# Kernel tuning notes

Measured on AMD Instinct MI355X. Metric: run time of the kernel, lower is better.

## Reference

```python
import jax, jax.numpy as jnp
import numpy as np

N_NODES = 100000
N_EDGES = 1600000
IN_DIM = 256
HID = 64
HEADS = 2
OUT_DIM = 256
NEG_SLOPE = 0.2  # DGL GATConv default


def setup_inputs() -> dict:
    key = jax.random.key(0)
    ks = jax.random.split(key, 10)
    feat = jax.random.normal(ks[0], (N_NODES, IN_DIM), dtype=jnp.float32)
    src = jax.random.randint(ks[1], (N_EDGES,), 0, N_NODES)
    dst = jax.random.randint(ks[2], (N_EDGES,), 0, N_NODES)
    W = jax.random.normal(ks[3], (IN_DIM, HEADS * HID), dtype=jnp.float32) * 0.05
    attn_l = jax.random.normal(ks[4], (HEADS, HID), dtype=jnp.float32) * 0.05
    attn_r = jax.random.normal(ks[5], (HEADS, HID), dtype=jnp.float32) * 0.05
    gat_bias = jnp.zeros((HEADS * HID,), dtype=jnp.float32)
    lin_W = jax.random.normal(ks[6], (HEADS * HID, OUT_DIM), dtype=jnp.float32) * 0.05
    lin_b = jnp.zeros((OUT_DIM,), dtype=jnp.float32)
    return {"feat": feat, "src": src, "dst": dst, "W": W, "attn_l": attn_l,
            "attn_r": attn_r, "gat_bias": gat_bias, "lin_W": lin_W, "lin_b": lin_b}


def reference(feat, src, dst, W, attn_l, attn_r, gat_bias, lin_W, lin_b):
    N = feat.shape[0]
    H, D = attn_l.shape
    # GATConv: linear projection -> [N, H, D]
    h = (feat @ W).reshape(N, H, D)
    el = jnp.sum(h * attn_l[None], axis=-1)  # [N, H]
    er = jnp.sum(h * attn_r[None], axis=-1)  # [N, H]
    # per-edge attention logits, LeakyReLU
    e = jax.nn.leaky_relu(el[src] + er[dst], NEG_SLOPE)  # [E, H]
    # edge softmax over incoming edges of each dst node
    m = jax.ops.segment_max(e, dst, num_segments=N)      # [N, H] (-inf for isolated nodes, unused)
    ee = jnp.exp(e - m[dst])
    s = jax.ops.segment_sum(ee, dst, num_segments=N)
    alpha = ee / s[dst]                                   # [E, H]
    # weighted aggregation: scatter-add messages to dst
    out = jax.ops.segment_sum(alpha[:, :, None] * h[src], dst, num_segments=N)  # [N, H, D]
    out = out + gat_bias.reshape(1, H, D)
    out = jax.nn.relu(out.reshape(N, H * D))
    return jax.nn.relu(out @ lin_W + lin_b)
```

## Files before the change

kernel.cpp:

```cpp
#include <hip/hip_runtime.h>

#define N_NODES 100000
#define N_EDGES 1600000
#define IN_DIM 256
#define HID 64
#define HEADS 2
#define HD 128
#define OUT_DIM 256
#define NEG_SLOPE 0.2f

typedef unsigned int uint32;
typedef unsigned short ushort16;
typedef __attribute__((ext_vector_type(8))) short bf16x8;
typedef __attribute__((ext_vector_type(4))) float f32x4;

__device__ __forceinline__ ushort16 f2bf(float f) {
    union { float f; uint32 u; } v; v.f = f;
    uint32 u = v.u;
    return (ushort16)((u + 0x7FFFu + ((u >> 16) & 1u)) >> 16);
}
__device__ __forceinline__ float bf2f(ushort16 b) {
    union { uint32 u; float f; } v; v.u = ((uint32)b) << 16;
    return v.f;
}
__device__ __forceinline__ float bflo(uint32 u) {
    union { uint32 u; float f; } v; v.u = u << 16;
    return v.f;
}
__device__ __forceinline__ float bfhi(uint32 u) {
    union { uint32 u; float f; } v; v.u = u & 0xffff0000u;
    return v.f;
}

__global__ __launch_bounds__(256)
void conv_w1(const float* __restrict__ W, ushort16* __restrict__ Wt)
{
    int idx = blockIdx.x * 256 + threadIdx.x;
    int n = idx >> 8, k = idx & 255;
    Wt[idx] = f2bf(W[k * HD + n]);
}
__global__ __launch_bounds__(256)
void conv_w2(const float* __restrict__ W, ushort16* __restrict__ Wt)
{
    int idx = blockIdx.x * 256 + threadIdx.x;
    int n = idx >> 7, k = idx & 127;
    Wt[idx] = f2bf(W[k * OUT_DIM + n]);
}

__global__ __launch_bounds__(256)
void gemm1_mfma(const float* __restrict__ A, const ushort16* __restrict__ Bt,
                ushort16* __restrict__ C, int M)
{
    __shared__ char alds[2 * 16384];
    const int t    = threadIdx.x;
    const int lane = t & 63;
    const int w    = t >> 6;
    const int wr   = w >> 1, wc = w & 1;
    const int m0   = blockIdx.x * 128;
    const int l15  = lane & 15;
    const int lq   = lane >> 4;

    f32x4 acc[4][4] = {};
    float4 av[8];

#define G1_LOAD(KT)                                                               \
    {                                                                             \
        _Pragma("unroll")                                                         \
        for (int i = 0; i < 8; i++) {                                             \
            int flat = t + i * 256;                                               \
            int r = flat >> 4, kq = (flat & 15) * 4;                              \
            int gr = m0 + r; if (gr >= M) gr = M - 1;                             \
            av[i] = *reinterpret_cast<const float4*>(                             \
                        &A[(size_t)gr * IN_DIM + (KT) * 64 + kq]);                \
        }                                                                         \
    }
#define G1_WRITE(BUF)                                                             \
    {                                                                             \
        _Pragma("unroll")                                                         \
        for (int i = 0; i < 8; i++) {                                             \
            int flat = t + i * 256;                                               \
            int r = flat >> 4, kq = (flat & 15) * 4;                              \
            uint2 p;                                                              \
            p.x = (uint32)f2bf(av[i].x) | ((uint32)f2bf(av[i].y) << 16);          \
            p.y = (uint32)f2bf(av[i].z) | ((uint32)f2bf(av[i].w) << 16);          \
            int byte = (r * 128 + kq * 2) ^ ((r & 7) << 4);                       \
            *reinterpret_cast<uint2*>(&alds[(BUF) * 16384 + byte]) = p;           \
        }                                                                         \
    }

    G1_LOAD(0); G1_WRITE(0);
    __syncthreads();
    int cur = 0;
    for (int kt = 0; kt < 4; kt++) {
        if (kt < 3) G1_LOAD(kt + 1);
        bf16x8 bfr[2][4];
#pragma unroll
        for (int ks = 0; ks < 2; ks++)
#pragma unroll
            for (int nf = 0; nf < 4; nf++) {
                int col = wc * 64 + nf * 16 + l15;
                int kb  = (kt * 2 + ks) * 32 + lq * 8;
                bfr[ks][nf] = *reinterpret_cast<const bf16x8*>(&Bt[(size_t)col * 256 + kb]);
            }
#pragma unroll
        for (int ks = 0; ks < 2; ks++) {
            bf16x8 afr[4];
#pragma unroll
            for (int mf = 0; mf < 4; mf++) {
                int row  = wr * 64 + mf * 16 + l15;
                int byte = (row * 128 + ks * 64 + lq * 16) ^ ((row & 7) << 4);
                afr[mf] = *reinterpret_cast<const bf16x8*>(&alds[cur * 16384 + byte]);
            }
#pragma unroll
            for (int mf = 0; mf < 4; mf++)
#pragma unroll
                for (int nf = 0; nf < 4; nf++)
                    acc[mf][nf] = __builtin_amdgcn_mfma_f32_16x16x32_bf16(
                        afr[mf], bfr[ks][nf], acc[mf][nf], 0, 0, 0);
        }
        if (kt < 3) G1_WRITE(cur ^ 1);
        __syncthreads();
        cur ^= 1;
    }
#pragma unroll
    for (int mf = 0; mf < 4; mf++)
#pragma unroll
        for (int nf = 0; nf < 4; nf++)
#pragma unroll
            for (int q = 0; q < 4; q++) {
                int row = m0 + wr * 64 + mf * 16 + lq * 4 + q;
                int col = wc * 64 + nf * 16 + l15;
                if (row < M) C[(size_t)row * HD + col] = f2bf(acc[mf][nf][q]);
            }
#undef G1_LOAD
#undef G1_WRITE
}

__global__ __launch_bounds__(256)
void gemm2_mfma(const ushort16* __restrict__ Ahi, const ushort16* __restrict__ Alo,
                const ushort16* __restrict__ Bt, const float* __restrict__ bias,
                float* __restrict__ Cout, int M)
{
    __shared__ char alds[2 * 32768];
    const int t    = threadIdx.x;
    const int lane = t & 63;
    const int w    = t >> 6;
    const int wr   = w >> 1, wc = w & 1;
    const int m0   = blockIdx.x * 128;
    const int n0   = blockIdx.y * 128;
    const int l15  = lane & 15;
    const int lq   = lane >> 4;

    f32x4 acc[4][4] = {};

#pragma unroll
    for (int p = 0; p < 2; p++) {
        const ushort16* src = p ? Alo : Ahi;
#pragma unroll
        for (int i = 0; i < 8; i++) {
            int flat = t + i * 256;
            int r = flat >> 4, e8 = (flat & 15) * 8;
            int gr = m0 + r; if (gr >= M) gr = M - 1;
            uint4 v = *reinterpret_cast<const uint4*>(&src[(size_t)gr * HD + e8]);
            int byte = (r * 256 + e8 * 2) ^ ((r & 7) << 4);
            *reinterpret_cast<uint4*>(&alds[p * 32768 + byte]) = v;
        }
    }
    bf16x8 bfr[4][4];
#pragma unroll
    for (int ks = 0; ks < 4; ks++)
#pragma unroll
        for (int nf = 0; nf < 4; nf++) {
            int col = n0 + wc * 64 + nf * 16 + l15;
            int kb  = ks * 32 + lq * 8;
            bfr[ks][nf] = *reinterpret_cast<const bf16x8*>(&Bt[(size_t)col * HD + kb]);
        }
    __syncthreads();

#pragma unroll
    for (int pass = 0; pass < 2; pass++) {
#pragma unroll
        for (int ks = 0; ks < 4; ks++) {
            bf16x8 afr[4];
#pragma unroll
            for (int mf = 0; mf < 4; mf++) {
                int row  = wr * 64 + mf * 16 + l15;
                int byte = (row * 256 + ks * 64 + lq * 16) ^ ((row & 7) << 4);
                afr[mf] = *reinterpret_cast<const bf16x8*>(&alds[pass * 32768 + byte]);
            }
#pragma unroll
            for (int mf = 0; mf < 4; mf++)
#pragma unroll
                for (int nf = 0; nf < 4; nf++)
                    acc[mf][nf] = __builtin_amdgcn_mfma_f32_16x16x32_bf16(
                        afr[mf], bfr[ks][nf], acc[mf][nf], 0, 0, 0);
        }
    }

    float bias_v[4];
#pragma unroll
    for (int nf = 0; nf < 4; nf++) bias_v[nf] = bias[n0 + wc * 64 + nf * 16 + l15];
#pragma unroll
    for (int mf = 0; mf < 4; mf++)
#pragma unroll
        for (int nf = 0; nf < 4; nf++)
#pragma unroll
            for (int q = 0; q < 4; q++) {
                int row = m0 + wr * 64 + mf * 16 + lq * 4 + q;
                int col = n0 + wc * 64 + nf * 16 + l15;
                if (row < M)
                    Cout[(size_t)row * OUT_DIM + col] = fmaxf(acc[mf][nf][q] + bias_v[nf], 0.f);
            }
}

__global__ __launch_bounds__(256)
void elr_kernel(const ushort16* __restrict__ hb, const float* __restrict__ attn_l,
                const float* __restrict__ attn_r, float* __restrict__ el,
                float* __restrict__ er)
{
    int w    = (int)((blockIdx.x * blockDim.x + threadIdx.x) >> 6);
    int lane = threadIdx.x & 63;
    if (w >= N_NODES) return;
    float h0 = bf2f(hb[(size_t)w * HD + lane]);
    float h1 = bf2f(hb[(size_t)w * HD + 64 + lane]);
    float v0 = h0 * attn_l[lane];
    float v1 = h1 * attn_l[64 + lane];
    float v2 = h0 * attn_r[lane];
    float v3 = h1 * attn_r[64 + lane];
#pragma unroll
    for (int o = 32; o; o >>= 1) {
        v0 += __shfl_xor(v0, o);
        v1 += __shfl_xor(v1, o);
        v2 += __shfl_xor(v2, o);
        v3 += __shfl_xor(v3, o);
    }
    if (lane == 0) {
        el[w * 2 + 0] = v0; el[w * 2 + 1] = v1;
        er[w * 2 + 0] = v2; er[w * 2 + 1] = v3;
    }
}

__global__ void deg_kernel(const int* __restrict__ dst, int* __restrict__ deg)
{
    int i = blockIdx.x * blockDim.x + threadIdx.x;
    if (i < N_EDGES) atomicAdd(&deg[dst[i]], 1);
}

#define SCAN_B 1024
#define SCAN_NB ((N_NODES + SCAN_B - 1) / SCAN_B)

__global__ __launch_bounds__(SCAN_B)
void scan_part(const int* __restrict__ deg, int* __restrict__ row_ptr,
               int* __restrict__ bsum)
{
    __shared__ int sdata[SCAN_B];
    const int t = threadIdx.x, b = blockIdx.x;
    const int i = b * SCAN_B + t;
    int v = (i < N_NODES) ? deg[i] : 0;
    sdata[t] = v;
    __syncthreads();
    for (int off = 1; off < SCAN_B; off <<= 1) {
        int x = 0;
        if (t >= off) x = sdata[t - off];
        __syncthreads();
        sdata[t] += x;
        __syncthreads();
    }
    if (i < N_NODES) row_ptr[i] = sdata[t] - v;
    if (t == SCAN_B - 1) bsum[b] = sdata[t];
}

__global__ __launch_bounds__(128)
void scan_top(int* __restrict__ bsum, int* __restrict__ row_ptr)
{
    __shared__ int sdata[128];
    const int t = threadIdx.x;
    int v = (t < SCAN_NB) ? bsum[t] : 0;
    sdata[t] = v;
    __syncthreads();
    for (int off = 1; off < 128; off <<= 1) {
        int x = 0;
        if (t >= off) x = sdata[t - off];
        __syncthreads();
        sdata[t] += x;
        __syncthreads();
    }
    if (t < SCAN_NB) bsum[t] = sdata[t] - v;
    if (t == 127) row_ptr[N_NODES] = sdata[127];
}

__global__ __launch_bounds__(SCAN_B)
void scan_add(int* __restrict__ row_ptr, const int* __restrict__ bsum)
{
    const int i = blockIdx.x * SCAN_B + threadIdx.x;
    if (i < N_NODES) row_ptr[i] += bsum[blockIdx.x];
}

__global__ void scatter_kernel(const int* __restrict__ src, const int* __restrict__ dst,
                               const int* __restrict__ row_ptr, int* __restrict__ cursor,
                               int* __restrict__ sorted_src)
{
    int i = blockIdx.x * blockDim.x + threadIdx.x;
    if (i < N_EDGES) {
        int d = dst[i];
        int p = row_ptr[d] + atomicAdd(&cursor[d], 1);
        sorted_src[p] = src[i];
    }
}

__global__ __launch_bounds__(256)
void node_kernel(const ushort16* __restrict__ hb, const float* __restrict__ el,
                 const float* __restrict__ er, const int* __restrict__ row_ptr,
                 const int* __restrict__ sorted_src, float* __restrict__ ws_e,
                 const float* __restrict__ gat_bias,
                 ushort16* __restrict__ agg_hi, ushort16* __restrict__ agg_lo)
{
    int n    = (int)((blockIdx.x * blockDim.x + threadIdx.x) >> 6);
    int lane = threadIdx.x & 63;
    if (n >= N_NODES) return;
    int beg = row_ptr[n], end = row_ptr[n + 1];

    float er0 = er[n * 2 + 0], er1 = er[n * 2 + 1];

    float mx0 = -1e30f, mx1 = -1e30f, s0 = 0.f, s1 = 0.f;
    for (int i = beg + lane; i < end; i += 64) {
        int s = sorted_src[i];
        float2 elv = *reinterpret_cast<const float2*>(&el[s * 2]);
        float e0 = elv.x + er0; e0 = e0 > 0.f ? e0 : NEG_SLOPE * e0;
        float e1 = elv.y + er1; e1 = e1 > 0.f ? e1 : NEG_SLOPE * e1;
        float2 st; st.x = e0; st.y = e1;
        *reinterpret_cast<float2*>(&ws_e[(size_t)i * 2]) = st;
        float m0n = fmaxf(mx0, e0);
        s0 = s0 * __expf(mx0 - m0n) + __expf(e0 - m0n);
        mx0 = m0n;
        float m1n = fmaxf(mx1, e1);
        s1 = s1 * __expf(mx1 - m1n) + __expf(e1 - m1n);
        mx1 = m1n;
    }
#pragma unroll
    for (int o = 32; o; o >>= 1) {
        float mo0 = __shfl_xor(mx0, o);
        float so0 = __shfl_xor(s0, o);
        float m0  = fmaxf(mx0, mo0);
        s0 = s0 * __expf(mx0 - m0) + so0 * __expf(mo0 - m0);
        mx0 = m0;
        float mo1 = __shfl_xor(mx1, o);
        float so1 = __shfl_xor(s1, o);
        float m1  = fmaxf(mx1, mo1);
        s1 = s1 * __expf(mx1 - m1) + so1 * __expf(mo1 - m1);
        mx1 = m1;
    }

    float inv0 = s0 > 0.f ? 1.f / s0 : 0.f;
    float inv1 = s1 > 0.f ? 1.f / s1 : 0.f;

    for (int i = beg + lane; i < end; i += 64) {
        float2 ev = *reinterpret_cast<const float2*>(&ws_e[(size_t)i * 2]);
        float2 av;
        av.x = __expf(ev.x - mx0) * inv0;
        av.y = __expf(ev.y - mx1) * inv1;
        *reinterpret_cast<float2*>(&ws_e[(size_t)i * 2]) = av;
    }
    __threadfence_block();

    const int slot = lane >> 4;
    const int j    = lane & 15;
    float acc[8] = {0.f, 0.f, 0.f, 0.f, 0.f, 0.f, 0.f, 0.f};

#define EDGE_BODY(E)                                                              \
    {                                                                             \
        float2 av = *reinterpret_cast<const float2*>(&ws_e[(size_t)(E) * 2]);     \
        int s = sorted_src[(E)];                                                  \
        float a = (j < 8) ? av.x : av.y;                                          \
        uint4 hv = *reinterpret_cast<const uint4*>(&hb[(size_t)s * HD + 8 * j]);  \
        acc[0] = fmaf(a, bflo(hv.x), acc[0]);                                     \
        acc[1] = fmaf(a, bfhi(hv.x), acc[1]);                                     \
        acc[2] = fmaf(a, bflo(hv.y), acc[2]);                                     \
        acc[3] = fmaf(a, bfhi(hv.y), acc[3]);                                     \
        acc[4] = fmaf(a, bflo(hv.z), acc[4]);                                     \
        acc[5] = fmaf(a, bfhi(hv.z), acc[5]);                                     \
        acc[6] = fmaf(a, bflo(hv.w), acc[6]);                                     \
        acc[7] = fmaf(a, bfhi(hv.w), acc[7]);                                     \
    }
    int e = beg + slot;
    for (; e + 4 < end; e += 8) { EDGE_BODY(e); EDGE_BODY(e + 4); }
    if (e < end) EDGE_BODY(e);
#undef EDGE_BODY

#pragma unroll
    for (int q = 0; q < 8; q++) {
        acc[q] += __shfl_xor(acc[q], 16);
        acc[q] += __shfl_xor(acc[q], 32);
    }

    if (lane < 16) {
        float4 b0 = *reinterpret_cast<const float4*>(&gat_bias[8 * j]);
        float4 b1 = *reinterpret_cast<const float4*>(&gat_bias[8 * j + 4]);
        float o[8];
        o[0] = fmaxf(acc[0] + b0.x, 0.f);
        o[1] = fmaxf(acc[1] + b0.y, 0.f);
        o[2] = fmaxf(acc[2] + b0.z, 0.f);
        o[3] = fmaxf(acc[3] + b0.w, 0.f);
        o[4] = fmaxf(acc[4] + b1.x, 0.f);
        o[5] = fmaxf(acc[5] + b1.y, 0.f);
        o[6] = fmaxf(acc[6] + b1.z, 0.f);
        o[7] = fmaxf(acc[7] + b1.w, 0.f);
        uint4 ph, pl;
        ushort16 hi[8], lo[8];
#pragma unroll
        for (int q = 0; q < 8; q++) {
            hi[q] = f2bf(o[q]);
            lo[q] = f2bf(o[q] - bf2f(hi[q]));
        }
        ph.x = (uint32)hi[0] | ((uint32)hi[1] << 16);
        ph.y = (uint32)hi[2] | ((uint32)hi[3] << 16);
        ph.z = (uint32)hi[4] | ((uint32)hi[5] << 16);
        ph.w = (uint32)hi[6] | ((uint32)hi[7] << 16);
        pl.x = (uint32)lo[0] | ((uint32)lo[1] << 16);
        pl.y = (uint32)lo[2] | ((uint32)lo[3] << 16);
        pl.z = (uint32)lo[4] | ((uint32)lo[5] << 16);
        pl.w = (uint32)lo[6] | ((uint32)lo[7] << 16);
        *reinterpret_cast<uint4*>(&agg_hi[(size_t)n * HD + 8 * j]) = ph;
        *reinterpret_cast<uint4*>(&agg_lo[(size_t)n * HD + 8 * j]) = pl;
    }
}

extern "C" void kernel_launch(void* const* d_in, const int* in_sizes, int n_in,
                              void* d_out, int out_size, void* d_ws, size_t ws_size,
                              hipStream_t stream)
{
    const float* feat     = (const float*)d_in[0];
    const int*   src      = (const int*)d_in[1];
    const int*   dst      = (const int*)d_in[2];
    const float* W        = (const float*)d_in[3];
    const float* attn_l   = (const float*)d_in[4];
    const float* attn_r   = (const float*)d_in[5];
    const float* gat_bias = (const float*)d_in[6];
    const float* lin_W    = (const float*)d_in[7];
    const float* lin_b    = (const float*)d_in[8];
    float* out = (float*)d_out;

    char* ws = (char*)d_ws;
    ushort16* hb     = (ushort16*)(ws + 0);
    ushort16* agg_hi = (ushort16*)(ws + 25600000);
    ushort16* agg_lo = (ushort16*)(ws + 51200000);
    float* ws_e   = (float*)(ws + 76800000);
    int*   ssrc   = (int*)  (ws + 89600000);
    float* el     = (float*)(ws + 96000000);
    float* er     = (float*)(ws + 96800000);
    int*   deg    = (int*)  (ws + 97600000);
    int*   cursor = (int*)  (ws + 98000000);
    int*   rowptr = (int*)  (ws + 98400000);
    int*   bsum   = (int*)  (ws + 98800128);
    ushort16* Wt1 = (ushort16*)(ws + 98804608);
    ushort16* Wt2 = (ushort16*)(ws + 98870144);

    hipMemsetAsync(deg, 0, 800000, stream);

    conv_w1<<<128, 256, 0, stream>>>(W, Wt1);
    conv_w2<<<128, 256, 0, stream>>>(lin_W, Wt2);

    dim3 blk(256);
    gemm1_mfma<<<(N_NODES + 127) / 128, blk, 0, stream>>>(feat, Wt1, hb, N_NODES);

    elr_kernel<<<(N_NODES + 3) / 4, 256, 0, stream>>>(hb, attn_l, attn_r, el, er);

    deg_kernel<<<(N_EDGES + 255) / 256, 256, 0, stream>>>(dst, deg);
    scan_part<<<SCAN_NB, SCAN_B, 0, stream>>>(deg, rowptr, bsum);
    scan_top<<<1, 128, 0, stream>>>(bsum, rowptr);
    scan_add<<<SCAN_NB, SCAN_B, 0, stream>>>(rowptr, bsum);
    scatter_kernel<<<(N_EDGES + 255) / 256, 256, 0, stream>>>(src, dst, rowptr, cursor, ssrc);

    node_kernel<<<(N_NODES + 3) / 4, 256, 0, stream>>>(hb, el, er, rowptr, ssrc, ws_e,
                                                       gat_bias, agg_hi, agg_lo);

    dim3 g2((N_NODES + 127) / 128, 2);
    gemm2_mfma<<<g2, blk, 0, stream>>>(agg_hi, agg_lo, Wt2, lin_b, out, N_NODES);
}
```

Before: 370.2 us.

## Compute edge softmax numerators in a parallel edge kernel with atomic denominators

The per-node max/sum/normalize passes in the aggregation kernel are replaced by a separate edge-parallel kernel. It computes exp(leaky_relu(el+er)) without max subtraction, writes the result to the dst-sorted position recorded by the scatter kernel, and atomically accumulates per-node denominators. The node kernel then only reads these unnormalized weights and scales by the reciprocal sum. The aim is to stop 64-lane waves from idling over short edge lists in the two extra passes. In exchange it adds a memset, float atomics and a position array, and it drops the numerical safeguard of max subtraction.

```diff
diff --git a/kernel.cpp b/kernel.cpp
--- a/kernel.cpp
+++ b/kernel.cpp
@@ -298,21 +298,42 @@
 
 __global__ void scatter_kernel(const int* __restrict__ src, const int* __restrict__ dst,
                                const int* __restrict__ row_ptr, int* __restrict__ cursor,
-                               int* __restrict__ sorted_src)
+                               int* __restrict__ sorted_src, int* __restrict__ pos)
 {
     int i = blockIdx.x * blockDim.x + threadIdx.x;
     if (i < N_EDGES) {
         int d = dst[i];
         int p = row_ptr[d] + atomicAdd(&cursor[d], 1);
         sorted_src[p] = src[i];
-    }
-}
-
-__global__ __launch_bounds__(256)
-void node_kernel(const ushort16* __restrict__ hb, const float* __restrict__ el,
-                 const float* __restrict__ er, const int* __restrict__ row_ptr,
-                 const int* __restrict__ sorted_src, float* __restrict__ ws_e,
-                 const float* __restrict__ gat_bias,
+        pos[i] = p;
+    }
+}
+
+__global__ __launch_bounds__(256)
+void edge_kernel(const int* __restrict__ src, const int* __restrict__ dst,
+                 const float* __restrict__ el, const float* __restrict__ er,
+                 const int* __restrict__ pos, float* __restrict__ ws_a,
+                 float* __restrict__ ssum)
+{
+    int i = blockIdx.x * 256 + threadIdx.x;
+    if (i >= N_EDGES) return;
+    int s = src[i], d = dst[i];
+    float2 elv = *reinterpret_cast<const float2*>(&el[2 * s]);
+    float2 erv = *reinterpret_cast<const float2*>(&er[2 * d]);
+    float e0 = elv.x + erv.x; e0 = e0 > 0.f ? e0 : NEG_SLOPE * e0;
+    float e1 = elv.y + erv.y; e1 = e1 > 0.f ? e1 : NEG_SLOPE * e1;
+    float ee0 = __expf(e0), ee1 = __expf(e1);
+    int p = pos[i];
+    float2 st; st.x = ee0; st.y = ee1;
+    *reinterpret_cast<float2*>(&ws_a[2 * p]) = st;
+    atomicAdd(&ssum[2 * d + 0], ee0);
+    atomicAdd(&ssum[2 * d + 1], ee1);
+}
+
+__global__ __launch_bounds__(256)
+void node_kernel(const ushort16* __restrict__ hb, const int* __restrict__ row_ptr,
+                 const int* __restrict__ sorted_src, const float* __restrict__ ws_a,
+                 const float* __restrict__ ssum, const float* __restrict__ gat_bias,
                  ushort16* __restrict__ agg_hi, ushort16* __restrict__ agg_lo)
 {
     int n    = (int)((blockIdx.x * blockDim.x + threadIdx.x) >> 6);
@@ -320,59 +341,24 @@
     if (n >= N_NODES) return;
     int beg = row_ptr[n], end = row_ptr[n + 1];
 
-    float er0 = er[n * 2 + 0], er1 = er[n * 2 + 1];
-
-    float mx0 = -1e30f, mx1 = -1e30f, s0 = 0.f, s1 = 0.f;
-    for (int i = beg + lane; i < end; i += 64) {
-        int s = sorted_src[i];
-        float2 elv = *reinterpret_cast<const float2*>(&el[s * 2]);
-        float e0 = elv.x + er0; e0 = e0 > 0.f ? e0 : NEG_SLOPE * e0;
-        float e1 = elv.y + er1; e1 = e1 > 0.f ? e1 : NEG_SLOPE * e1;
-        float2 st; st.x = e0; st.y = e1;
-        *reinterpret_cast<float2*>(&ws_e[(size_t)i * 2]) = st;
-        float m0n = fmaxf(mx0, e0);
-        s0 = s0 * __expf(mx0 - m0n) + __expf(e0 - m0n);
-        mx0 = m0n;
-        float m1n = fmaxf(mx1, e1);
-        s1 = s1 * __expf(mx1 - m1n) + __expf(e1 - m1n);
-        mx1 = m1n;
-    }
-#pragma unroll
-    for (int o = 32; o; o >>= 1) {
-        float mo0 = __shfl_xor(mx0, o);
-        float so0 = __shfl_xor(s0, o);
-        float m0  = fmaxf(mx0, mo0);
-        s0 = s0 * __expf(mx0 - m0) + so0 * __expf(mo0 - m0);
-        mx0 = m0;
-        float mo1 = __shfl_xor(mx1, o);
-        float so1 = __shfl_xor(s1, o);
-        float m1  = fmaxf(mx1, mo1);
-        s1 = s1 * __expf(mx1 - m1) + so1 * __expf(mo1 - m1);
-        mx1 = m1;
-    }
-
-    float inv0 = s0 > 0.f ? 1.f / s0 : 0.f;
-    float inv1 = s1 > 0.f ? 1.f / s1 : 0.f;
-
-    for (int i = beg + lane; i < end; i += 64) {
-        float2 ev = *reinterpret_cast<const float2*>(&ws_e[(size_t)i * 2]);
-        float2 av;
-        av.x = __expf(ev.x - mx0) * inv0;
-        av.y = __expf(ev.y - mx1) * inv1;
-        *reinterpret_cast<float2*>(&ws_e[(size_t)i * 2]) = av;
-    }
-    __threadfence_block();
-
     const int slot = lane >> 4;
     const int j    = lane & 15;
+    float2 sv = *reinterpret_cast<const float2*>(&ssum[2 * n]);
+    float inv0 = sv.x > 0.f ? 1.f / sv.x : 0.f;
+    float inv1 = sv.y > 0.f ? 1.f / sv.y : 0.f;
+    const float inv = (j < 8) ? inv0 : inv1;
+
+    const char*  hbase = (const char*)hb;
+    const uint32 joff  = (uint32)j << 4;
     float acc[8] = {0.f, 0.f, 0.f, 0.f, 0.f, 0.f, 0.f, 0.f};
 
 #define EDGE_BODY(E)                                                              \
     {                                                                             \
-        float2 av = *reinterpret_cast<const float2*>(&ws_e[(size_t)(E) * 2]);     \
+        float2 av = *reinterpret_cast<const float2*>(&ws_a[2 * (E)]);             \
         int s = sorted_src[(E)];                                                  \
-        float a = (j < 8) ? av.x : av.y;                                          \
-        uint4 hv = *reinterpret_cast<const uint4*>(&hb[(size_t)s * HD + 8 * j]);  \
+        float a = ((j < 8) ? av.x : av.y) * inv;                                  \
+        uint32 off = ((uint32)s << 8) | joff;                                     \
+        uint4 hv = *reinterpret_cast<const uint4*>(hbase + off);                  \
         acc[0] = fmaf(a, bflo(hv.x), acc[0]);                                     \
         acc[1] = fmaf(a, bfhi(hv.x), acc[1]);                                     \
         acc[2] = fmaf(a, bflo(hv.y), acc[2]);                                     \
@@ -443,13 +429,15 @@
     char* ws = (char*)d_ws;
     ushort16* hb     = (ushort16*)(ws + 0);
     ushort16* agg_hi = (ushort16*)(ws + 25600000);
+    int*      pos    = (int*)    (ws + 25600000);
     ushort16* agg_lo = (ushort16*)(ws + 51200000);
-    float* ws_e   = (float*)(ws + 76800000);
+    float* ws_a   = (float*)(ws + 76800000);
     int*   ssrc   = (int*)  (ws + 89600000);
     float* el     = (float*)(ws + 96000000);
     float* er     = (float*)(ws + 96800000);
     int*   deg    = (int*)  (ws + 97600000);
     int*   cursor = (int*)  (ws + 98000000);
+    float* ssum   = (float*)(ws + 97600000);
     int*   rowptr = (int*)  (ws + 98400000);
     int*   bsum   = (int*)  (ws + 98800128);
     ushort16* Wt1 = (ushort16*)(ws + 98804608);
@@ -469,9 +457,14 @@
     scan_part<<<SCAN_NB, SCAN_B, 0, stream>>>(deg, rowptr, bsum);
     scan_top<<<1, 128, 0, stream>>>(bsum, rowptr);
     scan_add<<<SCAN_NB, SCAN_B, 0, stream>>>(rowptr, bsum);
-    scatter_kernel<<<(N_EDGES + 255) / 256, 256, 0, stream>>>(src, dst, rowptr, cursor, ssrc);
-
-    node_kernel<<<(N_NODES + 3) / 4, 256, 0, stream>>>(hb, el, er, rowptr, ssrc, ws_e,
+    scatter_kernel<<<(N_EDGES + 255) / 256, 256, 0, stream>>>(src, dst, rowptr, cursor,
+                                                              ssrc, pos);
+
+    hipMemsetAsync(ssum, 0, 800000, stream);
+    edge_kernel<<<(N_EDGES + 255) / 256, 256, 0, stream>>>(src, dst, el, er, pos,
+                                                           ws_a, ssum);
+
+    node_kernel<<<(N_NODES + 3) / 4, 256, 0, stream>>>(hb, rowptr, ssrc, ws_a, ssum,
                                                        gat_bias, agg_hi, agg_lo);
 
     dim3 g2((N_NODES + 127) / 128, 2);
```

Result: slower. 545.2 us (+47.3%).
